# Kernel tuning notes

Measured on AMD Instinct MI355X. Metric: run time of the kernel, lower is better.

## Reference

```python
import jax, jax.numpy as jnp
import numpy as np

B, HT_, WT_, DM, C = 32, 32, 32, 768, 64  # batch, token grid, token dim, hough channels
THETA_RES, RHO_RES = 3, 1


def hough_transform(rows, cols, theta_res, rho_res):
    """Precompute binary vote matrix [rows*cols, n_rho*n_theta] (HT-LCNN style)."""
    theta = np.linspace(0.0, 180.0, int(np.ceil(180.0 / theta_res)) + 1)[:-1]
    w = theta.size                                # n_theta
    diag = np.sqrt((rows - 1) ** 2 + (cols - 1) ** 2)
    q = int(np.ceil(diag / rho_res))
    nrho = 2 * q + 1                              # n_rho
    cos_t, sin_t = np.cos(np.deg2rad(theta)), np.sin(np.deg2rad(theta))
    ii, jj = np.meshgrid(np.arange(rows), np.arange(cols), indexing='ij')
    xc = jj - cols / 2.0                          # centered pixel coords
    yc = rows / 2.0 - ii
    rho = xc[..., None] * cos_t + yc[..., None] * sin_t   # [rows, cols, w]
    ridx = np.round(rho / rho_res).astype(np.int64) + q
    tidx = np.broadcast_to(np.arange(w), ridx.shape)
    flat = (ridx * w + tidx).reshape(rows * cols, w)      # bin = rho_idx*w + theta_idx
    vote = np.zeros((rows * cols, nrho * w), dtype=np.float32)
    vote[np.arange(rows * cols)[:, None], flat] = 1.0
    return vote, nrho, w


def setup_inputs() -> dict:
    key = jax.random.key(0)
    ks = jax.random.split(key, 8)
    vote_np, n_rho, n_theta = hough_transform(HT_, WT_, THETA_RES, RHO_RES)
    ch = C // 2
    s = lambda n: 1.0 / np.sqrt(n)
    return dict(
        tokens=jax.random.normal(ks[0], (B, HT_ * WT_, DM), jnp.float32),
        vote=jnp.asarray(vote_np),                                    # [N, HR]
        Wt_in=jax.random.normal(ks[1], (C, DM), jnp.float32) * s(DM),   # to_feats 1x1
        bt_in=jnp.zeros((C,), jnp.float32),
        W1=jax.random.normal(ks[2], (ch, C), jnp.float32) * s(C),       # conv1 1x1 (no bias)
        W2=jax.random.normal(ks[3], (ch, ch, 9, 1), jnp.float32) * s(ch * 9),  # (9,1) conv on hough map
        W3=jax.random.normal(ks[4], (C, ch), jnp.float32) * s(ch),      # conv3 1x1 (no bias)
        Wt_out=jax.random.normal(ks[5], (DM, C), jnp.float32) * s(C),   # from_feats 1x1
        bt_out=jnp.zeros((DM,), jnp.float32),
        n_rho=n_rho,
        n_theta=n_theta,
    )


def reference(tokens, vote, Wt_in, bt_in, W1, W2, W3, Wt_out, bt_out, n_rho, n_theta):
    # tokens: [B, N, D]; vote: [N, HR] with HR = n_rho * n_theta.
    # 1x1 convs over the token grid are position-independent -> plain matmuls on [B, N, *].
    norm = jnp.clip(vote.sum(0), 1.0)                       # [HR] HT vote-count normalizer
    feat = tokens @ Wt_in.T + bt_in                         # [B, N, C]   (to_feats)
    y = jax.nn.relu(feat @ W1.T)                            # [B, N, ch]  (conv1 + relu)
    # HT: relu (idempotent here) + vote gather as dense matmul, normalized per hough bin
    ht = jnp.einsum('bnc,nh->bch', y, vote) / norm          # [B, ch, HR]
    bb, ch, hr = ht.shape
    ht = ht.reshape(bb, ch, n_rho, n_theta)                 # [B, ch, n_rho, n_theta]
    ht = jax.lax.conv_general_dilated(                      # (9,1) conv along rho, pad 4
        ht, W2, (1, 1), ((4, 4), (0, 0)),
        dimension_numbers=('NCHW', 'OIHW', 'NCHW'))
    # IHT: relu + transposed vote scatter, normalized by n_theta
    iht = jnp.einsum('bch,nh->bnc', jax.nn.relu(ht.reshape(bb, ch, hr)), vote) / n_theta
    z = iht @ W3.T                                          # [B, N, C]   (conv3)
    out = (feat + z) @ Wt_out.T + bt_out                    # residual + from_feats -> [B, N, D]
    return out
```

## Files before the change

### kernel.cpp

```cpp
#include <hip/hip_runtime.h>
#include <math.h>

#define NB    32
#define NTOK  1024
#define DMODEL 768
#define CF    64
#define CHH   32
#define NRHO  89
#define NTH   60
#define HRB   (NRHO*NTH)

typedef short bf16x8 __attribute__((ext_vector_type(8)));
typedef float f32x4  __attribute__((ext_vector_type(4)));
typedef unsigned int uint;
typedef unsigned short ushort;
typedef unsigned char uchar;

__device__ __forceinline__ ushort f2bf(float f) {
    uint u = __float_as_uint(f);
    return (ushort)((u + 0x7FFF + ((u >> 16) & 1)) >> 16);
}
__device__ __forceinline__ float bf2f(ushort u) {
    return __uint_as_float(((uint)u) << 16);
}
__device__ __forceinline__ uint cvtpk(float lo, float hi) {
    uint r;
    asm("v_cvt_pk_bf16_f32 %0, %1, %2" : "=v"(r) : "v"(lo), "v"(hi));
    return r;
}
__device__ __forceinline__ bf16x8 pack8(const float4& a, const float4& b) {
    uint4 u = make_uint4(cvtpk(a.x, a.y), cvtpk(a.z, a.w),
                         cvtpk(b.x, b.y), cvtpk(b.z, b.w));
    union { uint4 u4; bf16x8 v; } cv;
    cv.u4 = u;
    return cv.v;
}

__global__ __launch_bounds__(256) void k0_prep(
    int* __restrict__ perm, int* __restrict__ rowptr, uchar* __restrict__ rho8,
    const float* __restrict__ Wt_in, const float* __restrict__ bt_in,
    const float* __restrict__ W1, short* __restrict__ wcat,
    float* __restrict__ bcat,
    const float* __restrict__ Wt_out, const float* __restrict__ W2,
    short* __restrict__ wout, short* __restrict__ w2t) {
    __shared__ int rho_n[NTOK];
    __shared__ int cnt2[64 * 90];
    __shared__ int tot[96];
    __shared__ int base[96];
    __shared__ float w1row[64];
    const int tid = threadIdx.x;
    const int blk = blockIdx.x;

    if (blk < 60) {
        const int t = blk;
        const double rad = ((double)(t * 3)) * (M_PI / 180.0);
        const double ct = cos(rad), st = sin(rad);
        for (int n = tid; n < NTOK; n += 256) {
            int i = n >> 5, j = n & 31;
            double rho = (double)(j - 16) * ct + (double)(16 - i) * st;
            int ridx = (int)rint(rho) + 44;
            rho_n[n] = ridx;
            rho8[t * NTOK + n] = (uchar)ridx;
        }
        for (int i = tid; i < 64 * 90; i += 256) cnt2[i] = 0;
        __syncthreads();
        for (int n = tid; n < NTOK; n += 256)
            atomicAdd(&cnt2[(n >> 4) * 90 + rho_n[n]], 1);
        __syncthreads();
        if (tid < NRHO) {
            int s = 0;
            for (int c = 0; c < 64; ++c) {
                int v = cnt2[c * 90 + tid];
                cnt2[c * 90 + tid] = s;
                s += v;
            }
            tot[tid] = s;
        }
        __syncthreads();
        if (tid == 0) {
            int s = 0;
            for (int r = 0; r < NRHO; ++r) { base[r] = s; s += tot[r]; }
            base[NRHO] = s;
        }
        __syncthreads();
        if (tid < NRHO + 1) rowptr[t * 90 + tid] = base[tid];
        if (tid < 64) {
            const int c = tid;
            #pragma unroll
            for (int j = 0; j < 16; ++j) {
                int n = c * 16 + j;
                int r = rho_n[n];
                int cur = cnt2[c * 90 + r];
                cnt2[c * 90 + r] = cur + 1;
                perm[t * NTOK + base[r] + cur] = n;
            }
        }
    } else if (blk < 156) {
        const int c = blk - 60;
        if (c >= 64)
            for (int j = tid; j < 64; j += 256) w1row[j] = W1[(c - 64) * 64 + j];
        __syncthreads();
        for (int k = tid; k < DMODEL; k += 256) {
            float v;
            if (c < 64) v = Wt_in[c * DMODEL + k];
            else {
                v = 0.0f;
                for (int j = 0; j < 64; ++j) v += w1row[j] * Wt_in[j * DMODEL + k];
            }
            int kt = k >> 6, kk = k & 63;
            wcat[(((kt << 3) + (kk >> 3)) * 96 + c) * 8 + (k & 7)] = (short)f2bf(v);
        }
        if (tid == 0) {
            float bv;
            if (c < 64) bv = bt_in[c];
            else {
                bv = 0.0f;
                for (int j = 0; j < 64; ++j) bv += W1[(c - 64) * 64 + j] * bt_in[j];
            }
            bcat[c] = bv;
        }
    } else {
        int idx = (blk - 156) * 256 + tid;
        if (idx < 6144) {
            int d = idx >> 3, kg = idx & 7;
            float4 a = *(const float4*)&Wt_out[d * 64 + kg * 8];
            float4 b = *(const float4*)&Wt_out[d * 64 + kg * 8 + 4];
            uint4 v = make_uint4(cvtpk(a.x, a.y), cvtpk(a.z, a.w),
                                 cvtpk(b.x, b.y), cvtpk(b.z, b.w));
            *(uint4*)&wout[(((d >> 7) * 8 + kg) * 128 + (d & 127)) * 8] = v;
        } else if (idx < 6144 + 9216) {
            int q = idx - 6144;
            int e = q & 7, ln = (q >> 3) & 63, wm = (q >> 9) & 1, k = q >> 10;
            int o = wm * 16 + (ln & 15), i = ((ln >> 4) << 3) + e;
            w2t[q] = (short)f2bf(W2[(o * 32 + i) * 9 + k]);
        }
    }
}

__global__ __launch_bounds__(256, 4) void k1_mfma(
    const float* __restrict__ tokens, const short* __restrict__ wcat,
    const float* __restrict__ bcat, ushort* __restrict__ featb,
    ushort* __restrict__ ybb) {
    __shared__ ushort fs[128 * 64];
    __shared__ ushort ys[128 * 32];

    const int tid = threadIdx.x;
    const int lane = tid & 63, wave = tid >> 6;
    const int wm = wave >> 1, wn = wave & 1;
    const int row0 = blockIdx.x * 128;
    const int l15 = lane & 15, lq = lane >> 4;

    const float* aptr = tokens + (size_t)(row0 + wm * 64 + l15) * DMODEL + lq * 8;
    const short* bptr = wcat + ((size_t)lq * 96 + wn * 48 + l15) * 8;

    f32x4 acc[4][3] = {};

    for (int kt = 0; kt < 12; ++kt) {
        #pragma unroll
        for (int ks = 0; ks < 2; ++ks) {
            const float* ap = aptr + kt * 64 + ks * 32;
            bf16x8 av[4];
            #pragma unroll
            for (int i = 0; i < 4; ++i) {
                float4 lo = *(const float4*)&ap[(size_t)i * 16 * DMODEL];
                float4 hi = *(const float4*)&ap[(size_t)i * 16 * DMODEL + 4];
                av[i] = pack8(lo, hi);
            }
            const short* bp = bptr + ((size_t)(kt * 8 + ks * 4) * 96) * 8;
            bf16x8 bv[3];
            #pragma unroll
            for (int j = 0; j < 3; ++j)
                bv[j] = *(const bf16x8*)&bp[j * 16 * 8];
            #pragma unroll
            for (int i = 0; i < 4; ++i)
                #pragma unroll
                for (int j = 0; j < 3; ++j)
                    acc[i][j] = __builtin_amdgcn_mfma_f32_16x16x32_bf16(
                        av[i], bv[j], acc[i][j], 0, 0, 0);
        }
    }

    float bb[3];
    #pragma unroll
    for (int j = 0; j < 3; ++j) bb[j] = bcat[wn * 48 + j * 16 + l15];
    #pragma unroll
    for (int i = 0; i < 4; ++i) {
        #pragma unroll
        for (int j = 0; j < 3; ++j) {
            int c = wn * 48 + j * 16 + l15;
            int mlb = wm * 64 + i * 16 + (lq << 2);
            #pragma unroll
            for (int r = 0; r < 4; ++r) {
                float v = acc[i][j][r] + bb[j];
                if (c < 64) fs[(mlb + r) * 64 + c] = f2bf(v);
                else        ys[(mlb + r) * 32 + (c - 64)] = f2bf(fmaxf(v, 0.0f));
            }
        }
    }
    __syncthreads();
    for (int idx = tid; idx < 1024; idx += 256) {
        int ml = idx >> 3, cq = (idx & 7) * 8;
        *(uint4*)&featb[(size_t)(row0 + ml) * CF + cq] = *(const uint4*)&fs[ml * 64 + cq];
    }
    for (int idx = tid; idx < 512; idx += 256) {
        int ml = idx >> 2, cq = (idx & 3) * 8;
        *(uint4*)&ybb[(size_t)(row0 + ml) * CHH + cq] = *(const uint4*)&ys[ml * 32 + cq];
    }
}

__global__ __launch_bounds__(256) void k23_ht_conv(
    const ushort* __restrict__ ybb, const int* __restrict__ perm,
    const int* __restrict__ rowptr, const short* __restrict__ w2t,
    ushort* __restrict__ htcT) {
    __shared__ int pperm[NTOK];
    __shared__ int prow[90];
    __shared__ __align__(16) short insp[104 * 40];
    __shared__ uint outtu[NRHO * 18];

    const int tid = threadIdx.x;
    const int lane = tid & 63, wave = tid >> 6;
    const int wm = wave >> 1, wn = wave & 1;
    const int b = blockIdx.x / NTH, t = blockIdx.x % NTH;

    bf16x8 av[9];
    #pragma unroll
    for (int k = 0; k < 9; ++k)
        av[k] = *(const bf16x8*)&w2t[(((k * 2 + wm) * 64) + lane) * 8];

    for (int i = tid; i < NTOK; i += 256) pperm[i] = perm[t * NTOK + i];
    for (int i = tid; i < 90; i += 256) prow[i] = rowptr[t * 90 + i];
    for (int i = tid; i < 104 * 40 / 2; i += 256) ((uint*)insp)[i] = 0;
    __syncthreads();

    {
        const int c0 = (tid & 3) * 8, g = tid >> 2;
        const ushort* yp = ybb + (size_t)b * NTOK * CHH + c0;
        for (int rho = g; rho < NRHO; rho += 64) {
            int p0 = prow[rho], p1 = prow[rho + 1];
            float s0 = 0, s1 = 0, s2 = 0, s3 = 0, s4 = 0, s5 = 0, s6 = 0, s7 = 0;
            for (int k = p0; k < p1; ++k) {
                int n = pperm[k];
                uint4 v = *(const uint4*)&yp[n * CHH];
                s0 += bf2f((ushort)(v.x & 0xffff)); s1 += bf2f((ushort)(v.x >> 16));
                s2 += bf2f((ushort)(v.y & 0xffff)); s3 += bf2f((ushort)(v.y >> 16));
                s4 += bf2f((ushort)(v.z & 0xffff)); s5 += bf2f((ushort)(v.z >> 16));
                s6 += bf2f((ushort)(v.w & 0xffff)); s7 += bf2f((ushort)(v.w >> 16));
            }
            float iv = 1.0f / fmaxf((float)(p1 - p0), 1.0f);
            uint4 pk = make_uint4(cvtpk(s0 * iv, s1 * iv), cvtpk(s2 * iv, s3 * iv),
                                  cvtpk(s4 * iv, s5 * iv), cvtpk(s6 * iv, s7 * iv));
            *(uint4*)&insp[(rho + 4) * 40 + c0] = pk;
        }
    }
    __syncthreads();

    f32x4 acc[3] = {};
    #pragma unroll
    for (int f = 0; f < 3; ++f) {
        int Rn = wn * 48 + f * 16 + (lane & 15);
        #pragma unroll
        for (int k = 0; k < 9; ++k) {
            bf16x8 bv = *(const bf16x8*)&insp[(Rn + k) * 40 + ((lane >> 4) << 3)];
            acc[f] = __builtin_amdgcn_mfma_f32_16x16x32_bf16(av[k], bv, acc[f], 0, 0, 0);
        }
    }
    #pragma unroll
    for (int f = 0; f < 3; ++f) {
        int r = wn * 48 + f * 16 + (lane & 15);
        if (r < NRHO) {
            int ob = wm * 8 + ((lane >> 4) << 1);
            outtu[r * 18 + ob]     = cvtpk(fmaxf(acc[f][0], 0.0f), fmaxf(acc[f][1], 0.0f));
            outtu[r * 18 + ob + 1] = cvtpk(fmaxf(acc[f][2], 0.0f), fmaxf(acc[f][3], 0.0f));
        }
    }
    __syncthreads();

    {
        ushort* dst = htcT + (size_t)(b * NTH + t) * (NRHO * CHH);
        for (int idx = tid; idx < NRHO * 8; idx += 256) {
            int r = idx >> 3, q = idx & 7;
            uint2 v;
            v.x = outtu[r * 18 + q * 2];
            v.y = outtu[r * 18 + q * 2 + 1];
            *(uint2*)&dst[r * CHH + q * 4] = v;
        }
    }
}

__global__ __launch_bounds__(256, 4) void k45_iht_out(
    const ushort* __restrict__ htcT, const uchar* __restrict__ rho8,
    const float* __restrict__ W3, const ushort* __restrict__ featb,
    const short* __restrict__ wout, const float* __restrict__ bt_out,
    float* __restrict__ out) {
    __shared__ float w3t[32 * 64];
    __shared__ uchar lrho[NTH * 64];
    __shared__ float ihts[64 * 32];
    __shared__ __align__(16) short Alds[4096];

    const int tid = threadIdx.x;
    const int lane = tid & 63, wave = tid >> 6;
    const int wm = wave >> 1, wn = wave & 1;
    const int bid = blockIdx.x;
    const int b = bid >> 4;
    const int n0 = (bid & 15) * 64;
    const int l15 = lane & 15, lq = lane >> 4;

    for (int idx = tid; idx < 2048; idx += 256) {
        int c = idx >> 6, j = idx & 63;
        w3t[idx] = W3[j * 32 + c];
    }
    for (int idx = tid; idx < NTH * 64; idx += 256)
        lrho[idx] = rho8[(idx >> 6) * NTOK + n0 + (idx & 63)];
    __syncthreads();

    {
        const int c0 = (tid & 3) * 8, tok = tid >> 2;
        const ushort* hb = htcT + (size_t)b * NTH * NRHO * CHH + c0;
        float s[8] = {};
        #pragma unroll 6
        for (int t = 0; t < NTH; ++t) {
            int r = lrho[t * 64 + tok];
            uint4 v = *(const uint4*)&hb[(size_t)(t * NRHO + r) * CHH];
            s[0] += bf2f((ushort)(v.x & 0xffff)); s[1] += bf2f((ushort)(v.x >> 16));
            s[2] += bf2f((ushort)(v.y & 0xffff)); s[3] += bf2f((ushort)(v.y >> 16));
            s[4] += bf2f((ushort)(v.z & 0xffff)); s[5] += bf2f((ushort)(v.z >> 16));
            s[6] += bf2f((ushort)(v.w & 0xffff)); s[7] += bf2f((ushort)(v.w >> 16));
        }
        float4 r0, r1;
        r0.x = s[0] * (1.0f / 60.0f); r0.y = s[1] * (1.0f / 60.0f);
        r0.z = s[2] * (1.0f / 60.0f); r0.w = s[3] * (1.0f / 60.0f);
        r1.x = s[4] * (1.0f / 60.0f); r1.y = s[5] * (1.0f / 60.0f);
        r1.z = s[6] * (1.0f / 60.0f); r1.w = s[7] * (1.0f / 60.0f);
        *(float4*)&ihts[tok * 32 + c0] = r0;
        *(float4*)&ihts[tok * 32 + c0 + 4] = r1;
    }
    __syncthreads();

    {
        const int j = tid & 63, nb = tid >> 6;
        ushort* Au = (ushort*)Alds;
        for (int nn = nb; nn < 64; nn += 4) {
            float z = 0.0f;
            #pragma unroll 8
            for (int cc = 0; cc < 32; ++cc) z += ihts[nn * 32 + cc] * w3t[cc * 64 + j];
            float v = bf2f(featb[(size_t)(bid * 64 + nn) * CF + j]) + z;
            Au[((j >> 3) * 64 + nn) * 8 + (j & 7)] = f2bf(v);
        }
    }
    __syncthreads();

    const bf16x8* Ap = (const bf16x8*)Alds;
    bf16x8 avr[2][2];
    #pragma unroll
    for (int ks = 0; ks < 2; ++ks) {
        int kg = lq + ks * 4;
        #pragma unroll
        for (int i = 0; i < 2; ++i)
            avr[ks][i] = Ap[kg * 64 + wm * 32 + i * 16 + l15];
    }

    const short* bbase = wout + ((size_t)lq * 128 + wn * 64 + l15) * 8;
    for (int db = 0; db < 6; ++db) {
        f32x4 acc[2][4] = {};
        #pragma unroll
        for (int ks = 0; ks < 2; ++ks) {
            const short* bp = bbase + ((size_t)(db * 8 + ks * 4) * 128) * 8;
            bf16x8 bvv[4];
            #pragma unroll
            for (int jf = 0; jf < 4; ++jf)
                bvv[jf] = *(const bf16x8*)&bp[jf * 16 * 8];
            #pragma unroll
            for (int i = 0; i < 2; ++i)
                #pragma unroll
                for (int jf = 0; jf < 4; ++jf)
                    acc[i][jf] = __builtin_amdgcn_mfma_f32_16x16x32_bf16(
                        avr[ks][i], bvv[jf], acc[i][jf], 0, 0, 0);
        }
        const int d0 = db * 128 + wn * 64 + l15;
        float bb[4];
        #pragma unroll
        for (int jf = 0; jf < 4; ++jf) bb[jf] = bt_out[d0 + jf * 16];
        const int mrow = bid * 64 + wm * 32 + (lq << 2);
        #pragma unroll
        for (int i = 0; i < 2; ++i)
            #pragma unroll
            for (int r = 0; r < 4; ++r)
                #pragma unroll
                for (int jf = 0; jf < 4; ++jf)
                    out[(size_t)(mrow + i * 16 + r) * DMODEL + d0 + jf * 16] =
                        acc[i][jf][r] + bb[jf];
    }
}

extern "C" void kernel_launch(void* const* d_in, const int* in_sizes, int n_in,
                              void* d_out, int out_size, void* d_ws, size_t ws_size,
                              hipStream_t stream) {
    const float* tokens = (const float*)d_in[0];
    const float* Wt_in  = (const float*)d_in[2];
    const float* bt_in  = (const float*)d_in[3];
    const float* W1     = (const float*)d_in[4];
    const float* W2     = (const float*)d_in[5];
    const float* W3     = (const float*)d_in[6];
    const float* Wt_out = (const float*)d_in[7];
    const float* bt_out = (const float*)d_in[8];
    float* out = (float*)d_out;

    char* w = (char*)d_ws;
    int*    perm   = (int*)(w);
    int*    rowptr = (int*)(w + 245760);
    uchar*  rho8   = (uchar*)(w + 267360);
    short*  wcat   = (short*)(w + 328800);
    float*  bcat   = (float*)(w + 476256);
    short*  wout   = (short*)(w + 476640);
    short*  w2t    = (short*)(w + 574944);
    ushort* featb  = (ushort*)(w + 593376);
    ushort* ybb    = (ushort*)(w + 4787680);
    ushort* htcT   = (ushort*)(w + 6884832);

    k0_prep<<<216, 256, 0, stream>>>(perm, rowptr, rho8, Wt_in, bt_in, W1,
                                     wcat, bcat, Wt_out, W2, wout, w2t);
    k1_mfma<<<NB * NTOK / 128, 256, 0, stream>>>(tokens, wcat, bcat, featb, ybb);
    k23_ht_conv<<<NB * NTH, 256, 0, stream>>>(ybb, perm, rowptr, w2t, htcT);
    k45_iht_out<<<NB * (NTOK / 64), 256, 0, stream>>>(htcT, rho8, W3, featb,
                                                      wout, bt_out, out);
}
```

Baseline: 115.6 us.

## Shrink k1 row tile to 32 and register-prefetch next token slice

The first projection kernel now gives each block 32 token rows instead of 128, so it launches four times as many blocks (1024 instead of 256) and each wave holds one 16-row accumulator set instead of four. The main loop also loads the next k-slice of fp32 tokens into registers before the MFMAs of the current slice, a software prefetch that hides global load latency. This is meant to raise occupancy and memory-level parallelism on a bandwidth-bound read of the fp32 tokens. In exchange, each weight fragment is reused across fewer rows, so more weight traffic goes through the cache per row.

```diff
diff --git a/kernel.cpp b/kernel.cpp
--- a/kernel.cpp
+++ b/kernel.cpp
@@ -141,69 +141,69 @@
     const float* __restrict__ tokens, const short* __restrict__ wcat,
     const float* __restrict__ bcat, ushort* __restrict__ featb,
     ushort* __restrict__ ybb) {
-    __shared__ ushort fs[128 * 64];
-    __shared__ ushort ys[128 * 32];
+    __shared__ ushort fs[32 * 64];
+    __shared__ ushort ys[32 * 32];
 
     const int tid = threadIdx.x;
     const int lane = tid & 63, wave = tid >> 6;
     const int wm = wave >> 1, wn = wave & 1;
-    const int row0 = blockIdx.x * 128;
+    const int row0 = blockIdx.x * 32;
     const int l15 = lane & 15, lq = lane >> 4;
 
-    const float* aptr = tokens + (size_t)(row0 + wm * 64 + l15) * DMODEL + lq * 8;
+    const float* aptr = tokens + (size_t)(row0 + wm * 16 + l15) * DMODEL + lq * 8;
     const short* bptr = wcat + ((size_t)lq * 96 + wn * 48 + l15) * 8;
 
-    f32x4 acc[4][3] = {};
+    f32x4 acc[3] = {};
+
+    float4 c0 = *(const float4*)&aptr[0],  c1 = *(const float4*)&aptr[4];
+    float4 c2 = *(const float4*)&aptr[32], c3 = *(const float4*)&aptr[36];
 
     for (int kt = 0; kt < 12; ++kt) {
-        #pragma unroll
-        for (int ks = 0; ks < 2; ++ks) {
-            const float* ap = aptr + kt * 64 + ks * 32;
-            bf16x8 av[4];
-            #pragma unroll
-            for (int i = 0; i < 4; ++i) {
-                float4 lo = *(const float4*)&ap[(size_t)i * 16 * DMODEL];
-                float4 hi = *(const float4*)&ap[(size_t)i * 16 * DMODEL + 4];
-                av[i] = pack8(lo, hi);
-            }
-            const short* bp = bptr + ((size_t)(kt * 8 + ks * 4) * 96) * 8;
-            bf16x8 bv[3];
-            #pragma unroll
-            for (int j = 0; j < 3; ++j)
-                bv[j] = *(const bf16x8*)&bp[j * 16 * 8];
-            #pragma unroll
-            for (int i = 0; i < 4; ++i)
-                #pragma unroll
-                for (int j = 0; j < 3; ++j)
-                    acc[i][j] = __builtin_amdgcn_mfma_f32_16x16x32_bf16(
-                        av[i], bv[j], acc[i][j], 0, 0, 0);
-        }
+        float4 n0, n1, n2, n3;
+        if (kt < 11) {
+            const float* ap = aptr + (kt + 1) * 64;
+            n0 = *(const float4*)&ap[0];  n1 = *(const float4*)&ap[4];
+            n2 = *(const float4*)&ap[32]; n3 = *(const float4*)&ap[36];
+        }
+        bf16x8 a0 = pack8(c0, c1), a1 = pack8(c2, c3);
+        const short* bp0 = bptr + (size_t)(kt * 8) * 96 * 8;
+        const short* bp1 = bptr + (size_t)(kt * 8 + 4) * 96 * 8;
+        bf16x8 b0 = *(const bf16x8*)&bp0[0];
+        bf16x8 b1 = *(const bf16x8*)&bp0[16 * 8];
+        bf16x8 b2 = *(const bf16x8*)&bp0[32 * 8];
+        bf16x8 b3 = *(const bf16x8*)&bp1[0];
+        bf16x8 b4 = *(const bf16x8*)&bp1[16 * 8];
+        bf16x8 b5 = *(const bf16x8*)&bp1[32 * 8];
+        acc[0] = __builtin_amdgcn_mfma_f32_16x16x32_bf16(a0, b0, acc[0], 0, 0, 0);
+        acc[1] = __builtin_amdgcn_mfma_f32_16x16x32_bf16(a0, b1, acc[1], 0, 0, 0);
+        acc[2] = __builtin_amdgcn_mfma_f32_16x16x32_bf16(a0, b2, acc[2], 0, 0, 0);
+        acc[0] = __builtin_amdgcn_mfma_f32_16x16x32_bf16(a1, b3, acc[0], 0, 0, 0);
+        acc[1] = __builtin_amdgcn_mfma_f32_16x16x32_bf16(a1, b4, acc[1], 0, 0, 0);
+        acc[2] = __builtin_amdgcn_mfma_f32_16x16x32_bf16(a1, b5, acc[2], 0, 0, 0);
+        c0 = n0; c1 = n1; c2 = n2; c3 = n3;
     }
 
     float bb[3];
     #pragma unroll
     for (int j = 0; j < 3; ++j) bb[j] = bcat[wn * 48 + j * 16 + l15];
     #pragma unroll
-    for (int i = 0; i < 4; ++i) {
-        #pragma unroll
-        for (int j = 0; j < 3; ++j) {
-            int c = wn * 48 + j * 16 + l15;
-            int mlb = wm * 64 + i * 16 + (lq << 2);
-            #pragma unroll
-            for (int r = 0; r < 4; ++r) {
-                float v = acc[i][j][r] + bb[j];
-                if (c < 64) fs[(mlb + r) * 64 + c] = f2bf(v);
-                else        ys[(mlb + r) * 32 + (c - 64)] = f2bf(fmaxf(v, 0.0f));
-            }
-        }
-    }
-    __syncthreads();
-    for (int idx = tid; idx < 1024; idx += 256) {
-        int ml = idx >> 3, cq = (idx & 7) * 8;
+    for (int j = 0; j < 3; ++j) {
+        int c = wn * 48 + j * 16 + l15;
+        int mlb = wm * 16 + (lq << 2);
+        #pragma unroll
+        for (int r = 0; r < 4; ++r) {
+            float v = acc[j][r] + bb[j];
+            if (c < 64) fs[(mlb + r) * 64 + c] = f2bf(v);
+            else        ys[(mlb + r) * 32 + (c - 64)] = f2bf(fmaxf(v, 0.0f));
+        }
+    }
+    __syncthreads();
+    if (tid < 256) {
+        int ml = tid >> 3, cq = (tid & 7) * 8;
         *(uint4*)&featb[(size_t)(row0 + ml) * CF + cq] = *(const uint4*)&fs[ml * 64 + cq];
     }
-    for (int idx = tid; idx < 512; idx += 256) {
-        int ml = idx >> 2, cq = (idx & 3) * 8;
+    if (tid < 128) {
+        int ml = tid >> 2, cq = (tid & 3) * 8;
         *(uint4*)&ybb[(size_t)(row0 + ml) * CHH + cq] = *(const uint4*)&ys[ml * 32 + cq];
     }
 }
@@ -419,7 +419,7 @@
 
     k0_prep<<<216, 256, 0, stream>>>(perm, rowptr, rho8, Wt_in, bt_in, W1,
                                      wcat, bcat, Wt_out, W2, wout, w2t);
-    k1_mfma<<<NB * NTOK / 128, 256, 0, stream>>>(tokens, wcat, bcat, featb, ybb);
+    k1_mfma<<<NB * NTOK / 32, 256, 0, stream>>>(tokens, wcat, bcat, featb, ybb);
     k23_ht_conv<<<NB * NTH, 256, 0, stream>>>(ybb, perm, rowptr, w2t, htcT);
     k45_iht_out<<<NB * (NTOK / 64), 256, 0, stream>>>(htcT, rho8, W3, featb,
                                                       wout, bt_out, out);
```

Result: no change. 113.7 us (-1.6%).
